# Performance work log

Hardware: AMD Instinct MI355X
Metric: run time of the kernel (lower is better)

Reference implementation:

```python
import jax, jax.numpy as jnp
import numpy as np

N_NODES = 50000
N_EDGES = 800000


def setup_inputs() -> dict:
    key = jax.random.key(0)
    ks = jax.random.split(key, 6)
    x = jax.random.normal(ks[0], (N_NODES, 128), dtype=jnp.float32)
    edge_index = jax.random.randint(ks[1], (2, N_EDGES), 0, N_NODES, dtype=jnp.int64)
    # Glorot-ish scaled weights (PyG GCNConv uses glorot init)
    W1 = jax.random.normal(ks[2], (128, 256), dtype=jnp.float32) * (1.0 / np.sqrt(128))
    b1 = jnp.zeros((256,), dtype=jnp.float32)
    W2 = jax.random.normal(ks[3], (256, 128), dtype=jnp.float32) * (1.0 / np.sqrt(256))
    b2 = jnp.zeros((128,), dtype=jnp.float32)
    Wfc = jax.random.normal(ks[4], (128, 1), dtype=jnp.float32) * (1.0 / np.sqrt(128))
    bfc = jnp.zeros((1,), dtype=jnp.float32)
    return {"x": x, "edge_index": edge_index, "W1": W1, "b1": b1,
            "W2": W2, "b2": b2, "Wfc": Wfc, "bfc": bfc}


def _gcn_conv(x, src, dst, inv_sqrt_deg, W, b, n_nodes):
    # x: [N, Fin]; src/dst: [E+N] (self-loops included); W: [Fin, Fout]
    h = x @ W                                   # dense per-node transform
    norm = inv_sqrt_deg[src] * inv_sqrt_deg[dst]  # [E+N] symmetric normalization
    msg = h[src] * norm[:, None]                # gather + scale
    out = jax.ops.segment_sum(msg, dst, num_segments=n_nodes)  # scatter-add
    return out + b


def reference(x, edge_index, W1, b1, W2, b2, Wfc, bfc):
    n_nodes = x.shape[0]
    loops = jnp.arange(n_nodes, dtype=edge_index.dtype)
    src = jnp.concatenate([edge_index[0], loops])  # add self-loops (PyG default)
    dst = jnp.concatenate([edge_index[1], loops])
    deg = jax.ops.segment_sum(jnp.ones_like(dst, dtype=x.dtype), dst,
                              num_segments=n_nodes)  # in-degree incl. self-loop
    inv_sqrt_deg = jax.lax.rsqrt(deg)               # deg >= 1 due to self-loops

    h = jax.nn.relu(_gcn_conv(x, src, dst, inv_sqrt_deg, W1, b1, n_nodes))
    h = jax.nn.relu(_gcn_conv(h, src, dst, inv_sqrt_deg, W2, b2, n_nodes))
    pooled = jnp.mean(h, axis=0)                    # [output_dim]
    return pooled @ Wfc + bfc                       # [1]
```

## Files before the change

### kernel.cpp

```cpp
#include <hip/hip_runtime.h>


#define FEAT 128
#define TILE 4096
#define BSH  9
#define BKN  512

typedef __attribute__((ext_vector_type(8))) short short8;
typedef __attribute__((ext_vector_type(4))) float float4v;
typedef __attribute__((ext_vector_type(2))) float floatx2;

__device__ __forceinline__ unsigned int f2b(float f) {
    unsigned int u = __float_as_uint(f);
    return (u + 0x7fffu + ((u >> 16) & 1u)) >> 16;
}


__global__ __launch_bounds__(1024) void k_p1(const int* __restrict__ dst,
                                             int* __restrict__ cnt, int E, int B, int NW) {
    __shared__ int h[128];
    int t = threadIdx.x, w = blockIdx.x;
    if (t < B) h[t] = 0;
    __syncthreads();
    int e0 = w * TILE, e1 = min(e0 + TILE, E);
    for (int e = e0 + t; e < e1; e += 1024) atomicAdd(&h[dst[e] >> BSH], 1);
    __syncthreads();
    if (t < B) cnt[t * NW + w] = h[t];
}

__global__ __launch_bounds__(1024) void k_scanA(int* __restrict__ cnt,
                                                int* __restrict__ tot, int L) {
    __shared__ int s[1024];
    int t = threadIdx.x, g = blockIdx.x;
    int i = g * 1024 + t;
    int x = (i < L) ? cnt[i] : 0;
    s[t] = x;
    __syncthreads();
    for (int d = 1; d < 1024; d <<= 1) {
        int y = (t >= d) ? s[t - d] : 0;
        __syncthreads();
        s[t] += y;
        __syncthreads();
    }
    if (i < L) cnt[i] = s[t] - x;
    if (t == 1023) tot[g] = s[t];
}

__global__ void k_scanB(int* __restrict__ tot, int G) {
    __shared__ int s[64];
    int t = threadIdx.x;
    s[t] = (t < G) ? tot[t] : 0;
    __syncthreads();
    if (t == 0) {
        int run = 0;
        for (int g = 0; g < G; ++g) { int x = s[g]; s[g] = run; run += x; }
    }
    __syncthreads();
    if (t < G) tot[t] = s[t];
}

__global__ __launch_bounds__(1024) void k_p3(const int* __restrict__ src,
                                             const int* __restrict__ dst,
                                             const int* __restrict__ cnt,
                                             const int* __restrict__ tbase,
                                             unsigned int* __restrict__ ebuf,
                                             int E, int B, int NW) {
    __shared__ int cur[128];
    int t = threadIdx.x, w = blockIdx.x;
    if (t < B) { int i = t * NW + w; cur[t] = cnt[i] + tbase[i >> 10]; }
    __syncthreads();
    int e0 = w * TILE, e1 = min(e0 + TILE, E);
    for (int e = e0 + t; e < e1; e += 1024) {
        int d = dst[e], s = src[e];
        int p = atomicAdd(&cur[d >> BSH], 1);
        ebuf[p] = ((unsigned int)d << 16) | (unsigned int)s;
    }
}

__global__ __launch_bounds__(1024) void k_p4(const unsigned int* __restrict__ ebuf,
                                             const int* __restrict__ cnt,
                                             const int* __restrict__ tbase,
                                             float* __restrict__ isd,
                                             int* __restrict__ off,
                                             unsigned short* __restrict__ csr,
                                             int E, int B, int NW, int N) {
    __shared__ int h[BKN];
    __shared__ int s[BKN];
    __shared__ int cur[BKN];
    int t = threadIdx.x, b = blockIdx.x;
    if (t < BKN) h[t] = 0;
    __syncthreads();
    int i0 = b * NW;
    int s0 = cnt[i0] + tbase[i0 >> 10];
    int s1 = E;
    if (b + 1 < B) { int i1 = (b + 1) * NW; s1 = cnt[i1] + tbase[i1 >> 10]; }
    for (int e = s0 + t; e < s1; e += 1024)
        atomicAdd(&h[(ebuf[e] >> 16) & (BKN - 1)], 1);
    __syncthreads();
    int own = (t < BKN) ? h[t] : 0;
    if (t < BKN) s[t] = own;
    __syncthreads();
    for (int d = 1; d < BKN; d <<= 1) {
        int x = (t >= d && t < BKN) ? s[t - d] : 0;
        __syncthreads();
        if (t < BKN) s[t] += x;
        __syncthreads();
    }
    if (t < BKN) {
        int node = (b << BSH) + t;
        int myoff = s0 + s[t] - own;
        cur[t] = myoff;
        if (node < N) {
            isd[node] = rsqrtf((float)(own + 1));
            off[node] = myoff;
            if (node == N - 1) off[N] = s0 + s[t];
        }
    }
    __syncthreads();
    for (int e = s0 + t; e < s1; e += 1024) {
        unsigned int v = ebuf[e];
        int p = atomicAdd(&cur[(v >> 16) & (BKN - 1)], 1);
        csr[p] = (unsigned short)(v & 0xffffu);
    }
}


__device__ __forceinline__ void wswz_one(const float* W, unsigned short* out,
                                         int N, int tid) {
    int lane = tid & 63, f = tid >> 6;
    int NT = N >> 4;
    int nt = f % NT, kt = f / NT;
    int m = lane & 15, quad = lane >> 4;
    short8 pk;
#pragma unroll
    for (int j = 0; j < 8; ++j)
        pk[j] = (short)f2b(W[(size_t)(kt * 32 + quad * 8 + j) * N + nt * 16 + m]);
    *(short8*)(out + (size_t)tid * 8) = pk;
}

__global__ void k_prep(const float* __restrict__ x, const float* __restrict__ isd,
                       unsigned int* __restrict__ xq, float* __restrict__ pooled,
                       const float* __restrict__ W1, unsigned short* __restrict__ w1z,
                       const float* __restrict__ W2, unsigned short* __restrict__ w2z,
                       int total4) {
    int i = blockIdx.x * blockDim.x + threadIdx.x;
    if (i < 8192) pooled[i] = 0.f;
    if (i < 4096) wswz_one(W1, w1z, 256, i);
    else if (i < 8192) wswz_one(W2, w2z, 128, i - 4096);
    if (i >= total4) return;
    float w = isd[i >> 5] * 16.f;
    float4 v = ((const float4*)x)[i];
    unsigned int u = __builtin_amdgcn_cvt_pk_fp8_f32(v.x * w, v.y * w, 0u, false);
    u = __builtin_amdgcn_cvt_pk_fp8_f32(v.z * w, v.w * w, u, true);
    xq[i] = u;
}


__device__ __forceinline__ void gather_row(const unsigned short* __restrict__ Xq,
                                           const int* __restrict__ off,
                                           const unsigned short* __restrict__ csr,
                                           int wid, int lane, float& ra0, float& ra1) {
    int beg = off[wid], end = off[wid + 1];
    float a0, a1;
    {
        unsigned int q = Xq[(size_t)wid * 64 + lane];
        floatx2 f = __builtin_amdgcn_cvt_pk_f32_fp8(q, false);
        a0 = f[0]; a1 = f[1];
    }
    int e = beg;
    for (; e + 8 <= end; e += 8) {
        int s0 = csr[e],     s1 = csr[e + 1], s2 = csr[e + 2], s3 = csr[e + 3];
        int s4 = csr[e + 4], s5 = csr[e + 5], s6 = csr[e + 6], s7 = csr[e + 7];
        unsigned int q0 = Xq[(size_t)s0 * 64 + lane];
        unsigned int q1 = Xq[(size_t)s1 * 64 + lane];
        unsigned int q2 = Xq[(size_t)s2 * 64 + lane];
        unsigned int q3 = Xq[(size_t)s3 * 64 + lane];
        unsigned int q4 = Xq[(size_t)s4 * 64 + lane];
        unsigned int q5 = Xq[(size_t)s5 * 64 + lane];
        unsigned int q6 = Xq[(size_t)s6 * 64 + lane];
        unsigned int q7 = Xq[(size_t)s7 * 64 + lane];
        floatx2 f0 = __builtin_amdgcn_cvt_pk_f32_fp8(q0, false);
        floatx2 f1 = __builtin_amdgcn_cvt_pk_f32_fp8(q1, false);
        floatx2 f2 = __builtin_amdgcn_cvt_pk_f32_fp8(q2, false);
        floatx2 f3 = __builtin_amdgcn_cvt_pk_f32_fp8(q3, false);
        floatx2 f4 = __builtin_amdgcn_cvt_pk_f32_fp8(q4, false);
        floatx2 f5 = __builtin_amdgcn_cvt_pk_f32_fp8(q5, false);
        floatx2 f6 = __builtin_amdgcn_cvt_pk_f32_fp8(q6, false);
        floatx2 f7 = __builtin_amdgcn_cvt_pk_f32_fp8(q7, false);
        a0 += f0[0] + f1[0] + f2[0] + f3[0] + f4[0] + f5[0] + f6[0] + f7[0];
        a1 += f0[1] + f1[1] + f2[1] + f3[1] + f4[1] + f5[1] + f6[1] + f7[1];
    }
    for (; e + 2 <= end; e += 2) {
        int s0 = csr[e], s1 = csr[e + 1];
        unsigned int q0 = Xq[(size_t)s0 * 64 + lane];
        unsigned int q1 = Xq[(size_t)s1 * 64 + lane];
        floatx2 f0 = __builtin_amdgcn_cvt_pk_f32_fp8(q0, false);
        floatx2 f1 = __builtin_amdgcn_cvt_pk_f32_fp8(q1, false);
        a0 += f0[0] + f1[0];
        a1 += f0[1] + f1[1];
    }
    if (e < end) {
        unsigned int q0 = Xq[(size_t)csr[e] * 64 + lane];
        floatx2 f0 = __builtin_amdgcn_cvt_pk_f32_fp8(q0, false);
        a0 += f0[0];
        a1 += f0[1];
    }
    ra0 = a0; ra1 = a1;
}


__global__ __launch_bounds__(256) void k_agg1(const unsigned short* __restrict__ Xq,
                                              const int* __restrict__ off,
                                              const unsigned short* __restrict__ csr,
                                              const float* __restrict__ isd,
                                              unsigned int* __restrict__ out, int n) {
    int wid  = (blockIdx.x * 256 + threadIdx.x) >> 6;
    int lane = threadIdx.x & 63;
    if (wid >= n) return;
    wid = __builtin_amdgcn_readfirstlane(wid);
    float a0, a1;
    gather_row(Xq, off, csr, wid, lane, a0, a1);
    float wn = isd[wid] * 0.0625f;
    out[(size_t)wid * 64 + lane] = f2b(wn * a0) | (f2b(wn * a1) << 16);
}


__global__ __launch_bounds__(256) void k_gemm12(const unsigned short* __restrict__ A,
                                                const unsigned short* __restrict__ W1z,
                                                const float* __restrict__ b1,
                                                const unsigned short* __restrict__ W2z,
                                                const float* __restrict__ isd,
                                                unsigned char* __restrict__ t2q, int M) {
    __shared__ unsigned short h1s[64 * 272];
    int tid = threadIdx.x;
    int lane = tid & 63, wm = tid >> 6;
    int m = lane & 15, quad = lane >> 4;

    long arow = (long)blockIdx.x * 64 + wm * 16 + m;
    if (arow >= M) arow = M - 1;
    const short8* Ap  = (const short8*)(A + (size_t)arow * 128);
    const short8* W1p = (const short8*)W1z + lane;

    float4v acc1[16];
    float4v zero = {0.f, 0.f, 0.f, 0.f};
#pragma unroll
    for (int nt = 0; nt < 16; ++nt) acc1[nt] = zero;
#pragma unroll
    for (int kt = 0; kt < 4; ++kt) {
        short8 a = Ap[kt * 4 + quad];
#pragma unroll
        for (int nt = 0; nt < 16; ++nt)
            acc1[nt] = __builtin_amdgcn_mfma_f32_16x16x32_bf16(a, W1p[(kt * 16 + nt) * 64],
                                                               acc1[nt], 0, 0, 0);
    }
    int r0 = wm * 16 + quad * 4;
#pragma unroll
    for (int nt = 0; nt < 16; ++nt) {
        int col = nt * 16 + m;
        float bz = b1[col];
#pragma unroll
        for (int reg = 0; reg < 4; ++reg) {
            float v = fmaxf(acc1[nt][reg] + bz, 0.f);
            h1s[(r0 + reg) * 272 + col] = (unsigned short)f2b(v);
        }
    }
    __syncthreads();

    float4v acc2[8];
#pragma unroll
    for (int nt = 0; nt < 8; ++nt) acc2[nt] = zero;
    const short8* W2p = (const short8*)W2z + lane;
    int rloc = wm * 16 + m;
#pragma unroll
    for (int kt = 0; kt < 8; ++kt) {
        short8 a2 = *(const short8*)(h1s + rloc * 272 + kt * 32 + quad * 8);
#pragma unroll
        for (int nt = 0; nt < 8; ++nt)
            acc2[nt] = __builtin_amdgcn_mfma_f32_16x16x32_bf16(a2, W2p[(kt * 8 + nt) * 64],
                                                               acc2[nt], 0, 0, 0);
    }
    int gr0 = blockIdx.x * 64 + wm * 16 + quad * 4;
    float sc[4];
#pragma unroll
    for (int reg = 0; reg < 4; ++reg) {
        int r = gr0 + reg;
        sc[reg] = ((r < M) ? isd[r] : 0.f) * 16.f;
    }
#pragma unroll
    for (int nt = 0; nt < 8; ++nt) {
        int col = nt * 16 + m;
#pragma unroll
        for (int reg = 0; reg < 4; ++reg) {
            int gr = gr0 + reg;
            if (gr < M) {
                float v = acc2[nt][reg] * sc[reg];
                unsigned int b = __builtin_amdgcn_cvt_pk_fp8_f32(v, v, 0u, false);
                t2q[(size_t)gr * 128 + col] = (unsigned char)(b & 0xffu);
            }
        }
    }
}


__global__ __launch_bounds__(256) void k_agg2p(const unsigned short* __restrict__ Xq,
                                               const int* __restrict__ off,
                                               const unsigned short* __restrict__ csr,
                                               const float* __restrict__ isd,
                                               const float* __restrict__ b2,
                                               float* __restrict__ pooled, int n) {
    __shared__ float s0[256], s1[256];
    int tid = threadIdx.x;
    int wid  = (blockIdx.x * 256 + tid) >> 6;
    int lane = tid & 63;
    float r0 = 0.f, r1 = 0.f;
    if (wid < n) {
        int wu = __builtin_amdgcn_readfirstlane(wid);
        float a0, a1;
        gather_row(Xq, off, csr, wu, lane, a0, a1);
        float wn = isd[wu] * 0.0625f;
        r0 = fmaxf(wn * a0 + b2[2 * lane], 0.f);
        r1 = fmaxf(wn * a1 + b2[2 * lane + 1], 0.f);
    }
    s0[tid] = r0;
    s1[tid] = r1;
    __syncthreads();
    if (tid < 64) {
        float t0 = s0[tid] + s0[tid + 64] + s0[tid + 128] + s0[tid + 192];
        float t1 = s1[tid] + s1[tid + 64] + s1[tid + 128] + s1[tid + 192];
        float* dst = pooled + (blockIdx.x & 63) * 128;
        atomicAdd(&dst[2 * tid], t0);
        atomicAdd(&dst[2 * tid + 1], t1);
    }
}


__global__ void k_final(const float* __restrict__ pooled,
                        const float* __restrict__ Wfc,
                        const float* __restrict__ bfc,
                        float* __restrict__ out, float invN) {
    __shared__ float s[128];
    int t = threadIdx.x;
    float v = 0.f;
#pragma unroll
    for (int r = 0; r < 64; ++r) v += pooled[r * 128 + t];
    s[t] = v * invN * Wfc[t];
    __syncthreads();
    for (int d = 64; d > 0; d >>= 1) {
        if (t < d) s[t] += s[t + d];
        __syncthreads();
    }
    if (t == 0) out[0] = s[0] + bfc[0];
}


extern "C" void kernel_launch(void* const* d_in, const int* in_sizes, int n_in,
                              void* d_out, int out_size, void* d_ws, size_t ws_size,
                              hipStream_t stream) {
    const float* x   = (const float*)d_in[0];
    const int*   ei  = (const int*)d_in[1];
    const float* W1  = (const float*)d_in[2];
    const float* b1  = (const float*)d_in[3];
    const float* W2  = (const float*)d_in[4];
    const float* b2  = (const float*)d_in[5];
    const float* Wfc = (const float*)d_in[6];
    const float* bfc = (const float*)d_in[7];
    float* out = (float*)d_out;

    int N = in_sizes[0] / FEAT;
    int E = in_sizes[1] / 2;
    const int* src = ei;
    const int* dst = ei + E;

    int NW = (E + TILE - 1) / TILE;
    int B  = (N + BKN - 1) >> BSH;
    int L  = B * NW;
    int G  = (L + 1023) / 1024;

    char* p = (char*)d_ws;
    auto alloc = [&](size_t bytes) {
        char* r = p;
        p += (bytes + 255) & ~(size_t)255;
        return r;
    };
    int* cnt             = (int*)alloc((size_t)L * 4);
    int* tot             = (int*)alloc(64 * 4);
    unsigned int* ebuf   = (unsigned int*)alloc((size_t)E * 4);
    unsigned short* csr  = (unsigned short*)alloc((size_t)E * 2);
    float* isd           = (float*)alloc((size_t)N * 4);
    int* off             = (int*)alloc((size_t)(N + 1) * 4);
    unsigned int* xq     = (unsigned int*)alloc((size_t)N * 32 * 4);
    unsigned int* agg1b  = (unsigned int*)alloc((size_t)N * 64 * 4);
    unsigned char* t2q   = (unsigned char*)alloc((size_t)N * 128);
    unsigned short* w1z  = (unsigned short*)alloc(128 * 256 * 2);
    unsigned short* w2z  = (unsigned short*)alloc(256 * 128 * 2);
    float* pooled        = (float*)alloc(64 * 128 * 4);

    k_p1<<<NW, 1024, 0, stream>>>(dst, cnt, E, B, NW);
    k_scanA<<<G, 1024, 0, stream>>>(cnt, tot, L);
    k_scanB<<<1, 64, 0, stream>>>(tot, G);
    k_p3<<<NW, 1024, 0, stream>>>(src, dst, cnt, tot, ebuf, E, B, NW);
    k_p4<<<B, 1024, 0, stream>>>(ebuf, cnt, tot, isd, off, csr, E, B, NW, N);

    int total4 = N * FEAT / 4;
    k_prep<<<(total4 + 255) / 256, 256, 0, stream>>>(x, isd, xq, pooled,
                                                     W1, w1z, W2, w2z, total4);

    int gblk = (N + 63) / 64;
    int nblk = (N + 3) / 4;

    k_agg1<<<nblk, 256, 0, stream>>>((const unsigned short*)xq, off, csr, isd, agg1b, N);
    k_gemm12<<<gblk, 256, 0, stream>>>((const unsigned short*)agg1b, w1z, b1, w2z, isd, t2q, N);

    k_agg2p<<<nblk, 256, 0, stream>>>((const unsigned short*)t2q, off, csr, isd, b2,
                                      pooled, N);
    k_final<<<1, 128, 0, stream>>>(pooled, Wfc, bfc, out, 1.0f / (float)N);
}
```

Before: 199.6 us.

## Fold scanB and prep kernels into neighbouring CSR-build kernels

Removes two launches: the tiny top-level scan is recomputed redundantly per block inside k_p3 and k_p4, the weight swizzle and pooled zeroing move into k_p1, and the fp8 quantisation of x moves into k_p4 using the per-bucket inverse sqrt degrees kept in shared memory. This cuts launch and serialization overhead in a pipeline of many short kernels. In exchange k_p4 now runs with only B (~98) blocks, so the x quantisation pass over 25MB gets much less parallelism than the old wide launch.

```diff
diff --git a/kernel.cpp b/kernel.cpp
--- a/kernel.cpp
+++ b/kernel.cpp
@@ -16,12 +16,36 @@
 }
 
 
+__device__ __forceinline__ void wswz_one(const float* W, unsigned short* out,
+                                         int N, int tid) {
+    int lane = tid & 63, f = tid >> 6;
+    int NT = N >> 4;
+    int nt = f % NT, kt = f / NT;
+    int m = lane & 15, quad = lane >> 4;
+    short8 pk;
+#pragma unroll
+    for (int j = 0; j < 8; ++j)
+        pk[j] = (short)f2b(W[(size_t)(kt * 32 + quad * 8 + j) * N + nt * 16 + m]);
+    *(short8*)(out + (size_t)tid * 8) = pk;
+}
+
+
 __global__ __launch_bounds__(1024) void k_p1(const int* __restrict__ dst,
-                                             int* __restrict__ cnt, int E, int B, int NW) {
+                                             int* __restrict__ cnt,
+                                             const float* __restrict__ W1,
+                                             unsigned short* __restrict__ w1z,
+                                             const float* __restrict__ W2,
+                                             unsigned short* __restrict__ w2z,
+                                             float* __restrict__ pooled,
+                                             int E, int B, int NW) {
     __shared__ int h[128];
     int t = threadIdx.x, w = blockIdx.x;
     if (t < B) h[t] = 0;
     __syncthreads();
+    int gt = w * 1024 + t;
+    if (gt < 4096) wswz_one(W1, w1z, 256, gt);
+    else if (gt < 8192) wswz_one(W2, w2z, 128, gt - 4096);
+    if (gt < 8192) pooled[gt] = 0.f;
     int e0 = w * TILE, e1 = min(e0 + TILE, E);
     for (int e = e0 + t; e < e1; e += 1024) atomicAdd(&h[dst[e] >> BSH], 1);
     __syncthreads();
@@ -46,28 +70,23 @@
     if (t == 1023) tot[g] = s[t];
 }
 
-__global__ void k_scanB(int* __restrict__ tot, int G) {
-    __shared__ int s[64];
-    int t = threadIdx.x;
-    s[t] = (t < G) ? tot[t] : 0;
-    __syncthreads();
-    if (t == 0) {
-        int run = 0;
-        for (int g = 0; g < G; ++g) { int x = s[g]; s[g] = run; run += x; }
-    }
-    __syncthreads();
-    if (t < G) tot[t] = s[t];
-}
-
 __global__ __launch_bounds__(1024) void k_p3(const int* __restrict__ src,
                                              const int* __restrict__ dst,
                                              const int* __restrict__ cnt,
-                                             const int* __restrict__ tbase,
+                                             const int* __restrict__ tot,
                                              unsigned int* __restrict__ ebuf,
-                                             int E, int B, int NW) {
+                                             int E, int B, int NW, int G) {
     __shared__ int cur[128];
+    __shared__ int ctot[32];
     int t = threadIdx.x, w = blockIdx.x;
-    if (t < B) { int i = t * NW + w; cur[t] = cnt[i] + tbase[i >> 10]; }
+    if (t < G) ctot[t] = tot[t];
+    __syncthreads();
+    if (t == 0) {
+        int run = 0;
+        for (int g = 0; g < G; ++g) { int x = ctot[g]; ctot[g] = run; run += x; }
+    }
+    __syncthreads();
+    if (t < B) { int i = t * NW + w; cur[t] = cnt[i] + ctot[i >> 10]; }
     __syncthreads();
     int e0 = w * TILE, e1 = min(e0 + TILE, E);
     for (int e = e0 + t; e < e1; e += 1024) {
@@ -79,21 +98,31 @@
 
 __global__ __launch_bounds__(1024) void k_p4(const unsigned int* __restrict__ ebuf,
                                              const int* __restrict__ cnt,
-                                             const int* __restrict__ tbase,
+                                             const int* __restrict__ tot,
+                                             const float* __restrict__ x,
                                              float* __restrict__ isd,
                                              int* __restrict__ off,
                                              unsigned short* __restrict__ csr,
-                                             int E, int B, int NW, int N) {
+                                             unsigned int* __restrict__ xq,
+                                             int E, int B, int NW, int N, int G) {
     __shared__ int h[BKN];
     __shared__ int s[BKN];
     __shared__ int cur[BKN];
+    __shared__ float fisd[BKN];
+    __shared__ int ctot[32];
     int t = threadIdx.x, b = blockIdx.x;
+    if (t < G) ctot[t] = tot[t];
     if (t < BKN) h[t] = 0;
     __syncthreads();
+    if (t == 0) {
+        int run = 0;
+        for (int g = 0; g < G; ++g) { int x2 = ctot[g]; ctot[g] = run; run += x2; }
+    }
+    __syncthreads();
     int i0 = b * NW;
-    int s0 = cnt[i0] + tbase[i0 >> 10];
+    int s0 = cnt[i0] + ctot[i0 >> 10];
     int s1 = E;
-    if (b + 1 < B) { int i1 = (b + 1) * NW; s1 = cnt[i1] + tbase[i1 >> 10]; }
+    if (b + 1 < B) { int i1 = (b + 1) * NW; s1 = cnt[i1] + ctot[i1 >> 10]; }
     for (int e = s0 + t; e < s1; e += 1024)
         atomicAdd(&h[(ebuf[e] >> 16) & (BKN - 1)], 1);
     __syncthreads();
@@ -101,17 +130,20 @@
     if (t < BKN) s[t] = own;
     __syncthreads();
     for (int d = 1; d < BKN; d <<= 1) {
-        int x = (t >= d && t < BKN) ? s[t - d] : 0;
+        int y = (t >= d && t < BKN) ? s[t - d] : 0;
         __syncthreads();
-        if (t < BKN) s[t] += x;
+        if (t < BKN) s[t] += y;
         __syncthreads();
     }
+    int nb0 = b << BSH;
     if (t < BKN) {
-        int node = (b << BSH) + t;
+        int node = nb0 + t;
         int myoff = s0 + s[t] - own;
         cur[t] = myoff;
+        float fv = rsqrtf((float)(own + 1));
+        fisd[t] = fv;
         if (node < N) {
-            isd[node] = rsqrtf((float)(own + 1));
+            isd[node] = fv;
             off[node] = myoff;
             if (node == N - 1) off[N] = s0 + s[t];
         }
@@ -122,37 +154,17 @@
         int p = atomicAdd(&cur[(v >> 16) & (BKN - 1)], 1);
         csr[p] = (unsigned short)(v & 0xffffu);
     }
-}
-
-
-__device__ __forceinline__ void wswz_one(const float* W, unsigned short* out,
-                                         int N, int tid) {
-    int lane = tid & 63, f = tid >> 6;
-    int NT = N >> 4;
-    int nt = f % NT, kt = f / NT;
-    int m = lane & 15, quad = lane >> 4;
-    short8 pk;
-#pragma unroll
-    for (int j = 0; j < 8; ++j)
-        pk[j] = (short)f2b(W[(size_t)(kt * 32 + quad * 8 + j) * N + nt * 16 + m]);
-    *(short8*)(out + (size_t)tid * 8) = pk;
-}
-
-__global__ void k_prep(const float* __restrict__ x, const float* __restrict__ isd,
-                       unsigned int* __restrict__ xq, float* __restrict__ pooled,
-                       const float* __restrict__ W1, unsigned short* __restrict__ w1z,
-                       const float* __restrict__ W2, unsigned short* __restrict__ w2z,
-                       int total4) {
-    int i = blockIdx.x * blockDim.x + threadIdx.x;
-    if (i < 8192) pooled[i] = 0.f;
-    if (i < 4096) wswz_one(W1, w1z, 256, i);
-    else if (i < 8192) wswz_one(W2, w2z, 128, i - 4096);
-    if (i >= total4) return;
-    float w = isd[i >> 5] * 16.f;
-    float4 v = ((const float4*)x)[i];
-    unsigned int u = __builtin_amdgcn_cvt_pk_fp8_f32(v.x * w, v.y * w, 0u, false);
-    u = __builtin_amdgcn_cvt_pk_fp8_f32(v.z * w, v.w * w, u, true);
-    xq[i] = u;
+    int nfl4 = BKN * 32;
+    for (int j = t; j < nfl4; j += 1024) {
+        int node = nb0 + (j >> 5);
+        if (node < N) {
+            float w = fisd[j >> 5] * 16.f;
+            float4 v = ((const float4*)x)[(size_t)nb0 * 32 + j];
+            unsigned int u = __builtin_amdgcn_cvt_pk_fp8_f32(v.x * w, v.y * w, 0u, false);
+            u = __builtin_amdgcn_cvt_pk_fp8_f32(v.z * w, v.w * w, u, true);
+            xq[(size_t)nb0 * 32 + j] = u;
+        }
+    }
 }
 
 
@@ -395,15 +407,10 @@
     unsigned short* w2z  = (unsigned short*)alloc(256 * 128 * 2);
     float* pooled        = (float*)alloc(64 * 128 * 4);
 
-    k_p1<<<NW, 1024, 0, stream>>>(dst, cnt, E, B, NW);
+    k_p1<<<NW, 1024, 0, stream>>>(dst, cnt, W1, w1z, W2, w2z, pooled, E, B, NW);
     k_scanA<<<G, 1024, 0, stream>>>(cnt, tot, L);
-    k_scanB<<<1, 64, 0, stream>>>(tot, G);
-    k_p3<<<NW, 1024, 0, stream>>>(src, dst, cnt, tot, ebuf, E, B, NW);
-    k_p4<<<B, 1024, 0, stream>>>(ebuf, cnt, tot, isd, off, csr, E, B, NW, N);
-
-    int total4 = N * FEAT / 4;
-    k_prep<<<(total4 + 255) / 256, 256, 0, stream>>>(x, isd, xq, pooled,
-                                                     W1, w1z, W2, w2z, total4);
+    k_p3<<<NW, 1024, 0, stream>>>(src, dst, cnt, tot, ebuf, E, B, NW, G);
+    k_p4<<<B, 1024, 0, stream>>>(ebuf, cnt, tot, x, isd, off, csr, xq, E, B, NW, N, G);
 
     int gblk = (N + 63) / 64;
     int nblk = (N + 3) / 4;
```

Result: slower. 204.2 us (+2.3%).
